# Optimization experiments

Measured on AMD Instinct MI355X. Metric: run time of the kernel, lower is better.

Reference implementation:

```python
import jax, jax.numpy as jnp
import numpy as np

B, T, D, H, DH = 8, 1024, 512, 8, 64
DEPTH, V, FF = 8, 6400, 2048
NH, BS = 8, 64            # n_hashes, bucket_size
NB = T // BS              # 16 buckets
SELF_ATTN_VALUE = -5e4


def setup_inputs() -> dict:
    key = jax.random.key(0)
    ks = jax.random.split(key, 12)
    def n(k, shape, s=0.02):
        return jax.random.normal(k, shape, dtype=jnp.float32) * s
    return {
        "input_ids": jax.random.randint(ks[0], (B, T), 0, V),
        "token_emb": n(ks[1], (V, D)),
        "pos_emb": n(ks[2], (T, D)),
        "ln_attn_g": jnp.ones((DEPTH, D), jnp.float32),
        "ln_attn_b": jnp.zeros((DEPTH, D), jnp.float32),
        "Wqk": n(ks[3], (DEPTH, D, D)),
        "Wv": n(ks[4], (DEPTH, D, D)),
        "Wo": n(ks[5], (DEPTH, D, D)),
        "ln_ff_g": jnp.ones((DEPTH, D), jnp.float32),
        "ln_ff_b": jnp.zeros((DEPTH, D), jnp.float32),
        "W1": n(ks[6], (DEPTH, D, FF)),
        "b1": jnp.zeros((DEPTH, FF), jnp.float32),
        "W2": n(ks[7], (DEPTH, FF, D)),
        "b2": jnp.zeros((DEPTH, D), jnp.float32),
        "ln_f_g": jnp.ones((D,), jnp.float32),
        "ln_f_b": jnp.zeros((D,), jnp.float32),
        "Wfc": n(ks[8], (D, D)),
        # fixed random LSH rotation matrices, one per layer: [depth, dim_head, n_hashes, n_buckets//2]
        "rotations": jax.random.normal(ks[9], (DEPTH, DH, NH, NB // 2), dtype=jnp.float32),
    }


def layer_norm(x, g, b):
    m = jnp.mean(x, -1, keepdims=True)
    v = jnp.mean(jnp.square(x - m), -1, keepdims=True)
    return (x - m) * jax.lax.rsqrt(v + 1e-5) * g + b


def lsh_attention(x, Wqk, Wv, Wo, rot):
    """Reformer LSH self-attention: shared QK, NH hash rounds, bucket sort,
    chunked attention with 1-chunk look-back, multi-round logsumexp combine."""
    Bx = x.shape[0]
    qk = (x @ Wqk).reshape(Bx, T, H, DH).transpose(0, 2, 1, 3).reshape(Bx * H, T, DH)
    v = (x @ Wv).reshape(Bx, T, H, DH).transpose(0, 2, 1, 3).reshape(Bx * H, T, DH)

    # --- hashing: argmax over [rotated, -rotated] -> bucket ids per round ---
    rotated = jnp.einsum('btd,dhr->bhtr', qk, rot)                       # [BH,NH,T,NB/2]
    buckets = jnp.argmax(jnp.concatenate([rotated, -rotated], -1), -1)   # [BH,NH,T]
    buckets = buckets + (jnp.arange(NH) * NB)[None, :, None]
    buckets = buckets.reshape(Bx * H, NH * T)

    # --- stable sort by (bucket, position) ---
    ticker = jnp.arange(NH * T)
    b_t = buckets * T + (ticker % T)[None, :]
    sticker = jnp.argsort(b_t, axis=-1)
    undo = jnp.argsort(sticker, axis=-1)
    st = sticker % T                                                     # original positions
    sqk = jnp.take_along_axis(qk, st[..., None], axis=1)                 # [BH,NH*T,DH]
    sv = jnp.take_along_axis(v, st[..., None], axis=1)

    # --- chunk: NH*NB chunks of length BS, keys look back one chunk ---
    nc = NH * NB
    bq_t = st.reshape(-1, nc, BS)
    bq = sqk.reshape(-1, nc, BS, DH)
    bk = bq / (jnp.linalg.norm(bq, axis=-1, keepdims=True) + 1e-8)       # unit-length keys
    bv = sv.reshape(-1, nc, BS, DH)

    def look_back(t):
        return jnp.concatenate([t, jnp.roll(t, 1, axis=1)], axis=2)

    bk, bv, bkv_t = look_back(bk), look_back(bv), look_back(bq_t)

    dots = jnp.einsum('bnqd,bnkd->bnqk', bq, bk) * (DH ** -0.5)          # [BH,nc,BS,2BS]
    self_mask = bq_t[..., :, None] == bkv_t[..., None, :]
    dots = jnp.where(self_mask, SELF_ATTN_VALUE, dots)

    logits = jax.nn.logsumexp(dots, axis=-1, keepdims=True)
    probs = jnp.exp(dots - logits)
    bo = jnp.einsum('bnqk,bnkd->bnqd', probs, bv)

    # --- unsort and combine hash rounds weighted by per-round logsumexp ---
    so = bo.reshape(-1, NH * T, DH)
    slog = logits.reshape(-1, NH * T)
    o = jnp.take_along_axis(so, undo[..., None], axis=1).reshape(-1, NH, T, DH)
    lg = jnp.take_along_axis(slog, undo, axis=1).reshape(-1, NH, T, 1)
    w = jax.nn.softmax(lg, axis=1)
    out = jnp.sum(o * w, axis=1)                                         # [BH,T,DH]
    out = out.reshape(Bx, H, T, DH).transpose(0, 2, 1, 3).reshape(Bx, T, D)
    return out @ Wo


def reference(input_ids, token_emb, pos_emb, ln_attn_g, ln_attn_b, Wqk, Wv, Wo,
              ln_ff_g, ln_ff_b, W1, b1, W2, b2, ln_f_g, ln_f_b, Wfc, rotations):
    x = token_emb[input_ids] + pos_emb[None, :, :]
    # reversible residual streams: y1 = x1 + attn(norm(x2)); y2 = x2 + ff(norm(y1))
    x1, x2 = x, x
    for l in range(DEPTH):
        x1 = x1 + lsh_attention(layer_norm(x2, ln_attn_g[l], ln_attn_b[l]),
                                Wqk[l], Wv[l], Wo[l], rotations[l])
        h = layer_norm(x1, ln_ff_g[l], ln_ff_b[l])
        x2 = x2 + (jax.nn.gelu(h @ W1[l] + b1[l]) @ W2[l] + b2[l])
    x = 0.5 * (x1 + x2)
    x = layer_norm(x, ln_f_g, ln_f_b)
    return jnp.mean(x, axis=1) @ Wfc                                     # [B, embedding_dim]
```

## Files before the change

### kernel.cpp

```cpp
#include <hip/hip_runtime.h>
#include <hip/hip_bf16.h>
#include <cstdint>
#include <cstddef>

#define B_ 8
#define T_ 1024
#define D_ 512
#define H_ 8
#define DH_ 64
#define DEPTH_ 8
#define FF_ 2048
#define NH_ 8
#define BS_ 64
#define NB_ 16
#define NC_ 128
#define BH_ 64
#define ROWS_ 8192

typedef __attribute__((ext_vector_type(8))) short bf16x8;
typedef __attribute__((ext_vector_type(4))) float f32x4;

typedef __attribute__((address_space(1))) const unsigned int g_u32;
typedef __attribute__((address_space(3))) unsigned int l_u32;
__device__ __forceinline__ void gload16(const void* g, void* l) {
  __builtin_amdgcn_global_load_lds((g_u32*)g, (l_u32*)l, 16, 0, 0);
}

__device__ __forceinline__ float wave_sum(float v) {
#pragma unroll
  for (int o = 1; o < 64; o <<= 1) v += __shfl_xor(v, o);
  return v;
}

__device__ __forceinline__ float gelu_f(float u) {
  float c = u + 0.044715f * u * u * u;
  float t = tanhf(0.7978845608028654f * c);
  return 0.5f * u * (1.0f + t);
}

__global__ __launch_bounds__(128) void k_embed(const int* __restrict__ ids,
                                               const float* __restrict__ te,
                                               const float* __restrict__ pe,
                                               float* __restrict__ x1,
                                               float* __restrict__ x2) {
  int bt = blockIdx.x;
  int t = bt & (T_ - 1);
  int d = threadIdx.x * 4;
  int id = ids[bt];
  float4 v = *(const float4*)(te + (size_t)id * D_ + d);
  float4 p = *(const float4*)(pe + (size_t)t * D_ + d);
  v.x += p.x; v.y += p.y; v.z += p.z; v.w += p.w;
  *(float4*)(x1 + (size_t)bt * D_ + d) = v;
  *(float4*)(x2 + (size_t)bt * D_ + d) = v;
}

__global__ __launch_bounds__(256) void k_wt(const float* __restrict__ W,
                                            __hip_bfloat16* __restrict__ WT,
                                            int K, int N) {
  const float* Wl = W + (size_t)blockIdx.z * K * N;
  __hip_bfloat16* WTl = WT + (size_t)blockIdx.z * K * N;
  __shared__ float tile[32][33];
  int n0 = blockIdx.x * 32, k0 = blockIdx.y * 32;
  int tx = threadIdx.x & 31, ty = threadIdx.x >> 5;
#pragma unroll
  for (int i = 0; i < 32; i += 8)
    tile[ty + i][tx] = Wl[(size_t)(k0 + ty + i) * N + n0 + tx];
  __syncthreads();
#pragma unroll
  for (int i = 0; i < 32; i += 8)
    WTl[(size_t)(n0 + ty + i) * K + k0 + tx] = __float2bfloat16(tile[tx][ty + i]);
}

__global__ __launch_bounds__(256) void k_ln(const float* __restrict__ x,
                                            const float* __restrict__ xb,
                                            const float* __restrict__ g,
                                            const float* __restrict__ bb,
                                            float* __restrict__ y,
                                            __hip_bfloat16* __restrict__ yb) {
  int w = threadIdx.x >> 6, lane = threadIdx.x & 63;
  size_t row = (size_t)blockIdx.x * 4 + w;
  const float* xr = x + row * D_ + lane * 8;
  float v[8];
  *(float4*)(v)     = *(const float4*)(xr);
  *(float4*)(v + 4) = *(const float4*)(xr + 4);
  if (xb) {
    const float* x2r = xb + row * D_ + lane * 8;
    float u[8];
    *(float4*)(u)     = *(const float4*)(x2r);
    *(float4*)(u + 4) = *(const float4*)(x2r + 4);
#pragma unroll
    for (int i = 0; i < 8; ++i) v[i] = 0.5f * (v[i] + u[i]);
  }
  float s = 0.f;
#pragma unroll
  for (int i = 0; i < 8; ++i) s += v[i];
  s = wave_sum(s);
  float m = s * (1.0f / D_);
  float q = 0.f;
#pragma unroll
  for (int i = 0; i < 8; ++i) { float d = v[i] - m; q += d * d; }
  q = wave_sum(q);
  float inv = 1.0f / sqrtf(q * (1.0f / D_) + 1e-5f);
  float gg[8], bv[8];
  *(float4*)(gg)     = *(const float4*)(g + lane * 8);
  *(float4*)(gg + 4) = *(const float4*)(g + lane * 8 + 4);
  *(float4*)(bv)     = *(const float4*)(bb + lane * 8);
  *(float4*)(bv + 4) = *(const float4*)(bb + lane * 8 + 4);
  float o[8];
#pragma unroll
  for (int i = 0; i < 8; ++i) o[i] = (v[i] - m) * inv * gg[i] + bv[i];
  if (y) {
    float* yr = y + row * D_ + lane * 8;
    *(float4*)(yr)     = *(float4*)(o);
    *(float4*)(yr + 4) = *(float4*)(o + 4);
  }
  if (yb) {
    __hip_bfloat16 o16[8];
#pragma unroll
    for (int i = 0; i < 8; ++i) o16[i] = __float2bfloat16(o[i]);
    *(uint4*)(yb + row * D_ + lane * 8) = *(uint4*)o16;
  }
}

__global__ __launch_bounds__(256) void k_prep(const float* __restrict__ qkb,
                                              __hip_bfloat16* __restrict__ qsb,
                                              __hip_bfloat16* __restrict__ knb) {
  int w = threadIdx.x >> 6, lane = threadIdx.x & 63;
  size_t row = (size_t)blockIdx.x * 4 + w;
  const float* xr = qkb + row * D_ + lane * 8;
  float v[8];
  *(float4*)(v)     = *(const float4*)(xr);
  *(float4*)(v + 4) = *(const float4*)(xr + 4);
  float ss = 0.f;
#pragma unroll
  for (int i = 0; i < 8; ++i) ss += v[i] * v[i];
  ss += __shfl_xor(ss, 1); ss += __shfl_xor(ss, 2); ss += __shfl_xor(ss, 4);
  float inv = 1.0f / (sqrtf(ss) + 1e-8f);
  __hip_bfloat16 qo[8], ko[8];
#pragma unroll
  for (int i = 0; i < 8; ++i) {
    qo[i] = __float2bfloat16(v[i] * 0.125f);
    ko[i] = __float2bfloat16(v[i] * inv);
  }
  *(uint4*)(qsb + row * D_ + lane * 8) = *(uint4*)qo;
  *(uint4*)(knb + row * D_ + lane * 8) = *(uint4*)ko;
}

__global__ __launch_bounds__(256) void k_sgemm(const float* __restrict__ A,
                                               const float* __restrict__ Bm,
                                               float* __restrict__ C,
                                               int N, int K) {
  __shared__ float As[32][128];
  __shared__ float Bs[32][128];
  const int bn0 = blockIdx.x * 128;
  const int bm0 = blockIdx.y * 128;
  const int tid = threadIdx.x;
  const int w = tid >> 6, lane = tid & 63;
  const int wy = w >> 1, wx = w & 1;
  const int ly = lane >> 3, lx = lane & 7;
  const int rm = wy * 64 + ly * 8;
  const int cn = wx * 64 + lx * 8;
  float acc[8][8] = {};

  for (int k0 = 0; k0 < K; k0 += 32) {
#pragma unroll
    for (int ld = 0; ld < 4; ++ld) {
      int f = tid + ld * 256;
      int ar = f >> 3;
      int ac = (f & 7) << 2;
      float4 av = *(const float4*)(A + (size_t)(bm0 + ar) * K + k0 + ac);
      As[ac + 0][ar] = av.x; As[ac + 1][ar] = av.y;
      As[ac + 2][ar] = av.z; As[ac + 3][ar] = av.w;
      int br = f >> 5;
      int bc = (f & 31) << 2;
      *(float4*)(&Bs[br][bc]) = *(const float4*)(Bm + (size_t)(k0 + br) * N + bn0 + bc);
    }
    __syncthreads();
#pragma unroll
    for (int kk = 0; kk < 32; ++kk) {
      float a[8], b[8];
      *(float4*)(a)     = *(const float4*)(&As[kk][rm]);
      *(float4*)(a + 4) = *(const float4*)(&As[kk][rm + 4]);
      *(float4*)(b)     = *(const float4*)(&Bs[kk][cn]);
      *(float4*)(b + 4) = *(const float4*)(&Bs[kk][cn + 4]);
#pragma unroll
      for (int i = 0; i < 8; ++i)
#pragma unroll
        for (int j = 0; j < 8; ++j) acc[i][j] += a[i] * b[j];
    }
    __syncthreads();
  }
#pragma unroll
  for (int i = 0; i < 8; ++i) {
    float* crow = C + (size_t)(bm0 + rm + i) * N + bn0 + cn;
#pragma unroll
    for (int j0 = 0; j0 < 8; j0 += 4)
      *(float4*)(crow + j0) = make_float4(acc[i][j0], acc[i][j0 + 1], acc[i][j0 + 2], acc[i][j0 + 3]);
  }
}

template <int EPI>
__global__ __launch_bounds__(256) void k_bgemm(const __hip_bfloat16* __restrict__ A,
                                               const __hip_bfloat16* __restrict__ BT,
                                               const float* __restrict__ bias,
                                               void* __restrict__ Cv,
                                               int N, int K) {
  __shared__ __align__(16) __hip_bfloat16 As[128 * 32];
  __shared__ __align__(16) __hip_bfloat16 Bs[128 * 32];
  const int bn0 = blockIdx.x * 128;
  const int bm0 = blockIdx.y * 128;
  const int tid = threadIdx.x;
  const int w = tid >> 6, lane = tid & 63;
  const int wy = w >> 1, wx = w & 1;
  const int g = lane >> 4, lr = lane & 15;
  f32x4 acc[4][4] = {};

  const __hip_bfloat16* Abase = A + (size_t)bm0 * K;
  const __hip_bfloat16* Bbase = BT + (size_t)bn0 * K;

  for (int k0 = 0; k0 < K; k0 += 32) {
#pragma unroll
    for (int it = 0; it < 2; ++it) {
      int f = it * 256 + w * 64 + lane;
      int row = f >> 2;
      int kc = ((f & 3) ^ ((row >> 1) & 3)) << 3;
      gload16(Abase + (size_t)row * K + k0 + kc, &As[(it * 256 + w * 64) * 8]);
      gload16(Bbase + (size_t)row * K + k0 + kc, &Bs[(it * 256 + w * 64) * 8]);
    }
    __syncthreads();
    bf16x8 af[4], bfr[4];
#pragma unroll
    for (int m = 0; m < 4; ++m) {
      int row = wy * 64 + m * 16 + lr;
      af[m] = *(const bf16x8*)(&As[row * 32 + ((g ^ ((row >> 1) & 3)) << 3)]);
    }
#pragma unroll
    for (int n = 0; n < 4; ++n) {
      int row = wx * 64 + n * 16 + lr;
      bfr[n] = *(const bf16x8*)(&Bs[row * 32 + ((g ^ ((row >> 1) & 3)) << 3)]);
    }
#pragma unroll
    for (int m = 0; m < 4; ++m)
#pragma unroll
      for (int n = 0; n < 4; ++n)
        acc[m][n] = __builtin_amdgcn_mfma_f32_16x16x32_bf16(af[m], bfr[n], acc[m][n], 0, 0, 0);
    __syncthreads();
  }

  const int colb = bn0 + wx * 64 + lr;
  const int rowb = bm0 + wy * 64 + (g << 2);
#pragma unroll
  for (int m = 0; m < 4; ++m) {
#pragma unroll
    for (int n = 0; n < 4; ++n) {
      int c = colb + n * 16;
      int r0 = rowb + m * 16;
      float bsv = (EPI == 2 || EPI == 3) ? bias[c] : 0.f;
#pragma unroll
      for (int j = 0; j < 4; ++j) {
        float vlu = acc[m][n][j] + bsv;
        size_t idx = (size_t)(r0 + j) * N + c;
        if (EPI == 0) ((float*)Cv)[idx] = vlu;
        else if (EPI == 1) ((float*)Cv)[idx] += vlu;
        else if (EPI == 2) ((__hip_bfloat16*)Cv)[idx] = __float2bfloat16(gelu_f(vlu));
        else if (EPI == 3) ((float*)Cv)[idx] += vlu;
        else ((__hip_bfloat16*)Cv)[idx] = __float2bfloat16(vlu);
      }
    }
  }
}

__global__ __launch_bounds__(128) void k_bucket(const float* __restrict__ qk,
                                                const float* __restrict__ rotL,
                                                unsigned char* __restrict__ bkt) {
  int blk = blockIdx.x;
  int tc = blk & 7, h = (blk >> 3) & 7, b = blk >> 6;
  int t0 = tc << 7;
  __shared__ float qs[128][65];
  __shared__ float rs[4096];
  int tid = threadIdx.x;
  for (int f = tid; f < 4096; f += 128) rs[f] = rotL[f];
  const float* base = qk + ((size_t)(b * T_ + t0)) * D_ + h * DH_;
  for (int f = tid; f < 2048; f += 128) {
    int rw = f >> 4, c4 = (f & 15) << 2;
    float4 v = *(const float4*)(base + (size_t)rw * D_ + c4);
    qs[rw][c4] = v.x; qs[rw][c4 + 1] = v.y; qs[rw][c4 + 2] = v.z; qs[rw][c4 + 3] = v.w;
  }
  __syncthreads();
  float s[64];
#pragma unroll
  for (int jr = 0; jr < 64; ++jr) s[jr] = 0.f;
  for (int d = 0; d < 64; ++d) {
    float q = qs[tid][d];
    const float* rp = rs + d * 64;
#pragma unroll
    for (int j4 = 0; j4 < 16; ++j4) {
      float4 rv = *(const float4*)(rp + j4 * 4);
      s[j4 * 4 + 0] += q * rv.x; s[j4 * 4 + 1] += q * rv.y;
      s[j4 * 4 + 2] += q * rv.z; s[j4 * 4 + 3] += q * rv.w;
    }
  }
  int bh = b * H_ + h;
#pragma unroll
  for (int r = 0; r < 8; ++r) {
    float best = s[r * 8];
    int bi = 0;
#pragma unroll
    for (int idx = 1; idx < 16; ++idx) {
      float v = (idx < 8) ? s[r * 8 + idx] : -s[r * 8 + idx - 8];
      if (v > best) { best = v; bi = idx; }
    }
    bkt[((size_t)(bh * NH_ + r)) * T_ + t0 + tid] = (unsigned char)bi;
  }
}

__global__ __launch_bounds__(1024) void k_sort(const unsigned char* __restrict__ bkt,
                                               int* __restrict__ st,
                                               int* __restrict__ undo) {
  int r = blockIdx.x & 7, bh = blockIdx.x >> 3;
  int t = threadIdx.x;
  int bk = bkt[((size_t)(bh * NH_ + r)) * T_ + t];
  int w = t >> 6, lane = t & 63;
  __shared__ int cnt[16][16];
  __shared__ int off[16][16];
  __shared__ int tot[16];
  __shared__ int stt[16];
  unsigned long long below = (1ULL << lane) - 1ULL;
  int myrank = 0;
#pragma unroll
  for (int bb = 0; bb < 16; ++bb) {
    unsigned long long m = __ballot(bk == bb);
    if (bk == bb) myrank = __popcll(m & below);
    if (lane == 0) cnt[w][bb] = __popcll(m);
  }
  __syncthreads();
  if (t < 16) {
    int run = 0;
    for (int ww = 0; ww < 16; ++ww) { off[ww][t] = run; run += cnt[ww][t]; }
    tot[t] = run;
  }
  __syncthreads();
  if (t == 0) {
    int run = 0;
    for (int bb = 0; bb < 16; ++bb) { stt[bb] = run; run += tot[bb]; }
  }
  __syncthreads();
  int pos = stt[bk] + off[w][bk] + myrank;
  st[((size_t)(bh * NH_ + r)) * T_ + pos] = t;
  undo[((size_t)(bh * NH_ + r)) * T_ + t] = pos;
}

__global__ __launch_bounds__(256) void k_attn(const __hip_bfloat16* __restrict__ qs,
                                              const __hip_bfloat16* __restrict__ kn,
                                              const __hip_bfloat16* __restrict__ vv,
                                              const int* __restrict__ st,
                                              __hip_bfloat16* __restrict__ ob,
                                              float* __restrict__ lgb) {
  __shared__ __align__(16) __hip_bfloat16 Kb[128 * 72];
  __shared__ __align__(16) __hip_bfloat16 VbT[64 * 136];
  __shared__ __align__(16) __hip_bfloat16 PbQb[64 * 136];
  __shared__ int pos[128];

  const int c = blockIdx.x, bh = blockIdx.y;
  const int b = bh >> 3, h = bh & 7;
  const int r = c >> 4;
  const int pc = (c + NC_ - 1) & (NC_ - 1);
  const int tid = threadIdx.x;

  if (tid < 128) {
    int sc = (tid < 64) ? c : pc;
    int slot = ((sc & 15) << 6) + (tid & 63);
    pos[tid] = st[((size_t)(bh * NH_ + (sc >> 4))) * T_ + slot];
  }
  __syncthreads();

  const __hip_bfloat16* qbase = qs + ((size_t)b * T_) * D_ + h * DH_;
  const __hip_bfloat16* kbase = kn + ((size_t)b * T_) * D_ + h * DH_;
  const __hip_bfloat16* vbase = vv + ((size_t)b * T_) * D_ + h * DH_;

#pragma unroll
  for (int ld = 0; ld < 4; ++ld) {
    int f = ld * 256 + tid;
    int rw = f >> 3, c8 = (f & 7) << 3;
    *(uint4*)(&Kb[rw * 72 + c8]) = *(const uint4*)(kbase + (size_t)pos[rw] * D_ + c8);
  }
#pragma unroll
  for (int ld = 0; ld < 2; ++ld) {
    int f = ld * 256 + tid;
    int rw = f >> 3, c8 = (f & 7) << 3;
    *(uint4*)(&PbQb[rw * 72 + c8]) = *(const uint4*)(qbase + (size_t)pos[rw] * D_ + c8);
  }
  {
    const int w = tid >> 6, rl = tid & 7, d8 = (tid >> 3) & 7;
#pragma unroll
    for (int it = 0; it < 4; ++it) {
      int rw0 = it * 32 + w * 8;
      uint4 x = *(const uint4*)(vbase + (size_t)pos[rw0 + rl] * D_ + d8 * 8);
      unsigned short u[8];
      u[0] = x.x & 0xffff; u[1] = x.x >> 16;
      u[2] = x.y & 0xffff; u[3] = x.y >> 16;
      u[4] = x.z & 0xffff; u[5] = x.z >> 16;
      u[6] = x.w & 0xffff; u[7] = x.w >> 16;
#pragma unroll
      for (int k = 0; k < 3; ++k) {
        const int xm = 1 << k;
        const bool sel = (rl >> k) & 1;
#pragma unroll
        for (int j0 = 0; j0 < 8; ++j0) {
          if ((j0 >> k) & 1) continue;
          int j1 = j0 | (1 << k);
          unsigned int send = sel ? (unsigned int)u[j0] : (unsigned int)u[j1];
          unsigned int recv = (unsigned int)__shfl_xor((int)send, xm);
          if (sel) u[j0] = (unsigned short)recv; else u[j1] = (unsigned short)recv;
        }
      }
      int d = d8 * 8 + rl;
      uint4 y;
      y.x = (unsigned int)u[0] | ((unsigned int)u[1] << 16);
      y.y = (unsigned int)u[2] | ((unsigned int)u[3] << 16);
      y.z = (unsigned int)u[4] | ((unsigned int)u[5] << 16);
      y.w = (unsigned int)u[6] | ((unsigned int)u[7] << 16);
      *(uint4*)(&VbT[d * 136 + (rw0 ^ (((d >> 3) & 3) << 3))]) = y;
    }
  }
  __syncthreads();

  const int w = tid >> 6, lane = tid & 63;
  const int g = lane >> 4, l15 = lane & 15;
  const int q0 = w * 16;

  bf16x8 af0 = *(const bf16x8*)(&PbQb[(q0 + l15) * 72 + g * 8]);
  bf16x8 af1 = *(const bf16x8*)(&PbQb[(q0 + l15) * 72 + 32 + g * 8]);
  f32x4 dacc[8];
#pragma unroll
  for (int n = 0; n < 8; ++n) dacc[n] = (f32x4){0.f, 0.f, 0.f, 0.f};
#pragma unroll
  for (int n = 0; n < 8; ++n) {
    bf16x8 b0 = *(const bf16x8*)(&Kb[(n * 16 + l15) * 72 + g * 8]);
    bf16x8 b1 = *(const bf16x8*)(&Kb[(n * 16 + l15) * 72 + 32 + g * 8]);
    dacc[n] = __builtin_amdgcn_mfma_f32_16x16x32_bf16(af0, b0, dacc[n], 0, 0, 0);
    dacc[n] = __builtin_amdgcn_mfma_f32_16x16x32_bf16(af1, b1, dacc[n], 0, 0, 0);
  }
  __syncthreads();

  int qpos[4], kpos[8];
#pragma unroll
  for (int reg = 0; reg < 4; ++reg) qpos[reg] = pos[q0 + g * 4 + reg];
#pragma unroll
  for (int n = 0; n < 8; ++n) kpos[n] = pos[n * 16 + l15];
  float pr[8][4];
  float lgt[4];
#pragma unroll
  for (int reg = 0; reg < 4; ++reg) {
    float mx = -3.0e38f;
#pragma unroll
    for (int n = 0; n < 8; ++n) {
      float dv = dacc[n][reg];
      dv = (kpos[n] == qpos[reg]) ? -5.0e4f : dv;
      pr[n][reg] = dv;
      mx = fmaxf(mx, dv);
    }
    mx = fmaxf(mx, __shfl_xor(mx, 1));
    mx = fmaxf(mx, __shfl_xor(mx, 2));
    mx = fmaxf(mx, __shfl_xor(mx, 4));
    mx = fmaxf(mx, __shfl_xor(mx, 8));
    float s = 0.f;
#pragma unroll
    for (int n = 0; n < 8; ++n) { float e = __expf(pr[n][reg] - mx); pr[n][reg] = e; s += e; }
    s += __shfl_xor(s, 1); s += __shfl_xor(s, 2);
    s += __shfl_xor(s, 4); s += __shfl_xor(s, 8);
    lgt[reg] = mx + __logf(s);
    float isc = 1.0f / s;
#pragma unroll
    for (int n = 0; n < 8; ++n) pr[n][reg] *= isc;
  }
#pragma unroll
  for (int n = 0; n < 8; ++n)
#pragma unroll
    for (int reg = 0; reg < 4; ++reg)
      PbQb[(q0 + g * 4 + reg) * 136 + n * 16 + l15] = __float2bfloat16(pr[n][reg]);
  const size_t slotbase = ((size_t)(bh * NH_ + r)) * T_ + ((c & 15) << 6);
  if (l15 == 0) {
#pragma unroll
    for (int reg = 0; reg < 4; ++reg)
      lgb[slotbase + q0 + g * 4 + reg] = lgt[reg];
  }
  __syncthreads();

  bf16x8 va[4];
#pragma unroll
  for (int s = 0; s < 4; ++s) {
    int dd = w * 16 + l15;
    va[s] = *(const bf16x8*)(&VbT[dd * 136 + ((s * 32 + g * 8) ^ (((dd >> 3) & 3) << 3))]);
  }
#pragma unroll
  for (int n = 0; n < 4; ++n) {
    f32x4 oa = (f32x4){0.f, 0.f, 0.f, 0.f};
#pragma unroll
    for (int s = 0; s < 4; ++s) {
      bf16x8 pb = *(const bf16x8*)(&PbQb[(n * 16 + l15) * 136 + s * 32 + g * 8]);
      oa = __builtin_amdgcn_mfma_f32_16x16x32_bf16(va[s], pb, oa, 0, 0, 0);
    }
    int q = n * 16 + l15;
    int d = w * 16 + g * 4;
    __hip_bfloat16 o4[4];
#pragma unroll
    for (int reg = 0; reg < 4; ++reg) o4[reg] = __float2bfloat16(oa[reg]);
    *(uint2*)(&ob[(slotbase + q) * DH_ + d]) = *(uint2*)o4;
  }
}

__global__ __launch_bounds__(256) void k_combine(const __hip_bfloat16* __restrict__ ob,
                                                 const float* __restrict__ lgb,
                                                 const int* __restrict__ undo,
                                                 __hip_bfloat16* __restrict__ attnb) {
  int g = threadIdx.x >> 6, lane = threadIdx.x & 63;
  int idx = blockIdx.x * 4 + g;
  int bh = idx >> 10, t = idx & (T_ - 1);
  int b = bh >> 3, h = bh & 7;
  int su[8];
  float lg[8];
  float m = -3.0e38f;
#pragma unroll
  for (int r = 0; r < 8; ++r) {
    su[r] = undo[((size_t)(bh * NH_ + r)) * T_ + t];
    lg[r] = lgb[((size_t)(bh * NH_ + r)) * T_ + su[r]];
    m = fmaxf(m, lg[r]);
  }
  float s = 0.f;
#pragma unroll
  for (int r = 0; r < 8; ++r) { lg[r] = __expf(lg[r] - m); s += lg[r]; }
  float invs = 1.0f / s;
  float o = 0.f;
#pragma unroll
  for (int r = 0; r < 8; ++r)
    o += lg[r] * invs * __bfloat162float(ob[(((size_t)(bh * NH_ + r)) * T_ + su[r]) * DH_ + lane]);
  attnb[((size_t)(b * T_ + t)) * D_ + h * DH_ + lane] = __float2bfloat16(o);
}

__global__ void k_zero(float* __restrict__ p, int n) {
  int i = blockIdx.x * blockDim.x + threadIdx.x;
  if (i < n) p[i] = 0.f;
}

__global__ __launch_bounds__(256) void k_colsum(const float* __restrict__ xn,
                                                float* __restrict__ mean) {
  int b = blockIdx.x, dc = blockIdx.y, tc = blockIdx.z;
  int d = dc * 256 + threadIdx.x;
  float s = 0.f;
  for (int tt = 0; tt < 64; ++tt) {
    int t = tc * 64 + tt;
    s += xn[((size_t)(b * T_ + t)) * D_ + d];
  }
  atomicAdd(&mean[b * D_ + d], s);
}

__global__ __launch_bounds__(512) void k_fc(const float* __restrict__ mean,
                                            const float* __restrict__ Wfc,
                                            float* __restrict__ out) {
  int b = blockIdx.x, n = threadIdx.x;
  __shared__ float ms[512];
  ms[n] = mean[b * D_ + n] * (1.0f / 1024.0f);
  __syncthreads();
  float acc = 0.f;
  for (int d = 0; d < 512; ++d) acc += ms[d] * Wfc[(size_t)d * D_ + n];
  out[b * D_ + n] = acc;
}

extern "C" void kernel_launch(void* const* d_in, const int* in_sizes, int n_in,
                              void* d_out, int out_size, void* d_ws, size_t ws_size,
                              hipStream_t stream) {
  (void)in_sizes; (void)n_in; (void)out_size; (void)ws_size;
  const int*   ids  = (const int*)d_in[0];
  const float* te   = (const float*)d_in[1];
  const float* pe   = (const float*)d_in[2];
  const float* lag  = (const float*)d_in[3];
  const float* lab  = (const float*)d_in[4];
  const float* Wqk  = (const float*)d_in[5];
  const float* Wv   = (const float*)d_in[6];
  const float* Wo   = (const float*)d_in[7];
  const float* lfg  = (const float*)d_in[8];
  const float* lfb  = (const float*)d_in[9];
  const float* W1   = (const float*)d_in[10];
  const float* b1   = (const float*)d_in[11];
  const float* W2   = (const float*)d_in[12];
  const float* b2   = (const float*)d_in[13];
  const float* lnfg = (const float*)d_in[14];
  const float* lnfb = (const float*)d_in[15];
  const float* Wfc  = (const float*)d_in[16];
  const float* rot  = (const float*)d_in[17];

  char* ws = (char*)d_ws;
  size_t off = 0;
  auto carve = [&](size_t bytes) -> void* {
    void* p = ws + off;
    off += (bytes + 255) & ~(size_t)255;
    return p;
  };
  float* x1    = (float*)carve((size_t)ROWS_ * D_ * 4);
  float* x2    = (float*)carve((size_t)ROWS_ * D_ * 4);
  float* xn    = (float*)carve((size_t)ROWS_ * D_ * 4);
  float* qkb   = (float*)carve((size_t)ROWS_ * D_ * 4);
  __hip_bfloat16* vvb   = (__hip_bfloat16*)carve((size_t)ROWS_ * D_ * 2);
  __hip_bfloat16* qsb   = (__hip_bfloat16*)carve((size_t)ROWS_ * D_ * 2);
  __hip_bfloat16* knb   = (__hip_bfloat16*)carve((size_t)ROWS_ * D_ * 2);
  __hip_bfloat16* xnb   = (__hip_bfloat16*)carve((size_t)ROWS_ * D_ * 2);
  __hip_bfloat16* attnb = (__hip_bfloat16*)carve((size_t)ROWS_ * D_ * 2);
  __hip_bfloat16* ob    = (__hip_bfloat16*)carve((size_t)BH_ * NH_ * T_ * DH_ * 2);
  __hip_bfloat16* hid   = ob;
  unsigned char* bkt = (unsigned char*)carve((size_t)BH_ * NH_ * T_);
  int*   stb   = (int*)carve((size_t)BH_ * NH_ * T_ * 4);
  int*   undo  = (int*)carve((size_t)BH_ * NH_ * T_ * 4);
  float* lgb   = (float*)carve((size_t)BH_ * NH_ * T_ * 4);
  float* meanb = (float*)carve((size_t)B_ * D_ * 4);
  __hip_bfloat16* WvT = (__hip_bfloat16*)carve((size_t)DEPTH_ * D_ * D_ * 2);
  __hip_bfloat16* WoT = (__hip_bfloat16*)carve((size_t)DEPTH_ * D_ * D_ * 2);
  __hip_bfloat16* W1T = (__hip_bfloat16*)carve((size_t)DEPTH_ * D_ * FF_ * 2);
  __hip_bfloat16* W2T = (__hip_bfloat16*)carve((size_t)DEPTH_ * FF_ * D_ * 2);

  k_wt<<<dim3(D_ / 32, D_ / 32, DEPTH_), 256, 0, stream>>>(Wv, WvT, D_, D_);
  k_wt<<<dim3(D_ / 32, D_ / 32, DEPTH_), 256, 0, stream>>>(Wo, WoT, D_, D_);
  k_wt<<<dim3(FF_ / 32, D_ / 32, DEPTH_), 256, 0, stream>>>(W1, W1T, D_, FF_);
  k_wt<<<dim3(D_ / 32, FF_ / 32, DEPTH_), 256, 0, stream>>>(W2, W2T, FF_, D_);

  k_embed<<<ROWS_, 128, 0, stream>>>(ids, te, pe, x1, x2);

  for (int l = 0; l < DEPTH_; ++l) {
    const float* wqk = Wqk + (size_t)l * D_ * D_;
    const __hip_bfloat16* wvt = WvT + (size_t)l * D_ * D_;
    const __hip_bfloat16* wot = WoT + (size_t)l * D_ * D_;
    const __hip_bfloat16* w1t = W1T + (size_t)l * D_ * FF_;
    const __hip_bfloat16* w2t = W2T + (size_t)l * FF_ * D_;

    k_ln<<<ROWS_ / 4, 256, 0, stream>>>(x2, nullptr, lag + l * D_, lab + l * D_, xn, xnb);
    k_sgemm<<<dim3(D_ / 128, ROWS_ / 128), 256, 0, stream>>>(xn, wqk, qkb, D_, D_);
    k_bgemm<4><<<dim3(D_ / 128, ROWS_ / 128), 256, 0, stream>>>(xnb, wvt, nullptr, vvb, D_, D_);
    k_prep<<<ROWS_ / 4, 256, 0, stream>>>(qkb, qsb, knb);
    k_bucket<<<512, 128, 0, stream>>>(qkb, rot + (size_t)l * 4096, bkt);
    k_sort<<<512, 1024, 0, stream>>>(bkt, stb, undo);
    k_attn<<<dim3(NC_, BH_), 256, 0, stream>>>(qsb, knb, vvb, stb, ob, lgb);
    k_combine<<<BH_ * T_ / 4, 256, 0, stream>>>(ob, lgb, undo, attnb);
    k_bgemm<1><<<dim3(D_ / 128, ROWS_ / 128), 256, 0, stream>>>(attnb, wot, nullptr, x1, D_, D_);

    k_ln<<<ROWS_ / 4, 256, 0, stream>>>(x1, nullptr, lfg + l * D_, lfb + l * D_, nullptr, xnb);
    k_bgemm<2><<<dim3(FF_ / 128, ROWS_ / 128), 256, 0, stream>>>(xnb, w1t, b1 + l * FF_, hid, FF_, D_);
    k_bgemm<3><<<dim3(D_ / 128, ROWS_ / 128), 256, 0, stream>>>(hid, w2t, b2 + l * D_, x2, D_, FF_);
  }

  k_ln<<<ROWS_ / 4, 256, 0, stream>>>(x1, x2, lnfg, lnfb, xn, nullptr);
  k_zero<<<16, 256, 0, stream>>>(meanb, B_ * D_);
  k_colsum<<<dim3(B_, 2, 16), 256, 0, stream>>>(xn, meanb);
  k_fc<<<B_, 512, 0, stream>>>(meanb, Wfc, (float*)d_out);
}
```

Baseline: 3.200 ms.

## Replace fp32 QK GEMM with split-bf16 MFMA GEMM and drop softmax max-subtraction

The fp32 SIMT GEMM for the shared QK projection is replaced with a three-term split-bf16 (hi/lo) MFMA GEMM. The layernorm now also emits the bf16 residual, and a new transpose kernel splits Wqk into hi and lo parts. This keeps near-fp32 accuracy, which the hashing argmax needs, while using the matrix cores. Separately, the attention softmax drops its max reduction and applies the 1/sum normalization after the PV matmul through shared memory. That relies on the scaled logits being small enough not to overflow exp.

```diff
diff --git a/kernel.cpp b/kernel.cpp
--- a/kernel.cpp
+++ b/kernel.cpp
@@ -71,12 +71,38 @@
     WTl[(size_t)(n0 + ty + i) * K + k0 + tx] = __float2bfloat16(tile[tx][ty + i]);
 }
 
+__global__ __launch_bounds__(256) void k_wt2(const float* __restrict__ W,
+                                             __hip_bfloat16* __restrict__ WhT,
+                                             __hip_bfloat16* __restrict__ WlT,
+                                             int K, int N) {
+  const float* Wl = W + (size_t)blockIdx.z * K * N;
+  __hip_bfloat16* WhTl = WhT + (size_t)blockIdx.z * K * N;
+  __hip_bfloat16* WlTl = WlT + (size_t)blockIdx.z * K * N;
+  __shared__ float tile[32][33];
+  int n0 = blockIdx.x * 32, k0 = blockIdx.y * 32;
+  int tx = threadIdx.x & 31, ty = threadIdx.x >> 5;
+#pragma unroll
+  for (int i = 0; i < 32; i += 8)
+    tile[ty + i][tx] = Wl[(size_t)(k0 + ty + i) * N + n0 + tx];
+  __syncthreads();
+#pragma unroll
+  for (int i = 0; i < 32; i += 8) {
+    float v = tile[tx][ty + i];
+    __hip_bfloat16 hi = __float2bfloat16(v);
+    float lo = v - __bfloat162float(hi);
+    size_t idx = (size_t)(n0 + ty + i) * K + k0 + tx;
+    WhTl[idx] = hi;
+    WlTl[idx] = __float2bfloat16(lo);
+  }
+}
+
 __global__ __launch_bounds__(256) void k_ln(const float* __restrict__ x,
                                             const float* __restrict__ xb,
                                             const float* __restrict__ g,
                                             const float* __restrict__ bb,
                                             float* __restrict__ y,
-                                            __hip_bfloat16* __restrict__ yb) {
+                                            __hip_bfloat16* __restrict__ yb,
+                                            __hip_bfloat16* __restrict__ ylo) {
   int w = threadIdx.x >> 6, lane = threadIdx.x & 63;
   size_t row = (size_t)blockIdx.x * 4 + w;
   const float* xr = x + row * D_ + lane * 8;
@@ -119,7 +145,88 @@
 #pragma unroll
     for (int i = 0; i < 8; ++i) o16[i] = __float2bfloat16(o[i]);
     *(uint4*)(yb + row * D_ + lane * 8) = *(uint4*)o16;
-  }
+    if (ylo) {
+      __hip_bfloat16 l16[8];
+#pragma unroll
+      for (int i = 0; i < 8; ++i)
+        l16[i] = __float2bfloat16(o[i] - __bfloat162float(o16[i]));
+      *(uint4*)(ylo + row * D_ + lane * 8) = *(uint4*)l16;
+    }
+  }
+}
+
+__global__ __launch_bounds__(256) void k_qgemm(const __hip_bfloat16* __restrict__ Ah,
+                                               const __hip_bfloat16* __restrict__ Al,
+                                               const __hip_bfloat16* __restrict__ BhT,
+                                               const __hip_bfloat16* __restrict__ BlT,
+                                               float* __restrict__ C, int N, int K) {
+  __shared__ __align__(16) __hip_bfloat16 Ash[128 * 32];
+  __shared__ __align__(16) __hip_bfloat16 Asl[128 * 32];
+  __shared__ __align__(16) __hip_bfloat16 Bsh[128 * 32];
+  __shared__ __align__(16) __hip_bfloat16 Bsl[128 * 32];
+  const int bn0 = blockIdx.x * 128;
+  const int bm0 = blockIdx.y * 128;
+  const int tid = threadIdx.x;
+  const int w = tid >> 6, lane = tid & 63;
+  const int wy = w >> 1, wx = w & 1;
+  const int g = lane >> 4, lr = lane & 15;
+  f32x4 acc[4][4] = {};
+  const size_t aoff = (size_t)bm0 * K;
+  const size_t boff = (size_t)bn0 * K;
+
+  for (int k0 = 0; k0 < K; k0 += 32) {
+#pragma unroll
+    for (int it = 0; it < 2; ++it) {
+      int f = it * 256 + w * 64 + lane;
+      int row = f >> 2;
+      int kc = ((f & 3) ^ ((row >> 1) & 3)) << 3;
+      size_t ga = aoff + (size_t)row * K + k0 + kc;
+      size_t gb = boff + (size_t)row * K + k0 + kc;
+      int lo = (it * 256 + w * 64) * 8;
+      gload16(Ah + ga, &Ash[lo]);
+      gload16(Al + ga, &Asl[lo]);
+      gload16(BhT + gb, &Bsh[lo]);
+      gload16(BlT + gb, &Bsl[lo]);
+    }
+    __syncthreads();
+    bf16x8 ah[4], al[4], bh[4], bl[4];
+#pragma unroll
+    for (int m = 0; m < 4; ++m) {
+      int row = wy * 64 + m * 16 + lr;
+      int o = row * 32 + ((g ^ ((row >> 1) & 3)) << 3);
+      ah[m] = *(const bf16x8*)(&Ash[o]);
+      al[m] = *(const bf16x8*)(&Asl[o]);
+    }
+#pragma unroll
+    for (int n = 0; n < 4; ++n) {
+      int row = wx * 64 + n * 16 + lr;
+      int o = row * 32 + ((g ^ ((row >> 1) & 3)) << 3);
+      bh[n] = *(const bf16x8*)(&Bsh[o]);
+      bl[n] = *(const bf16x8*)(&Bsl[o]);
+    }
+#pragma unroll
+    for (int m = 0; m < 4; ++m)
+#pragma unroll
+      for (int n = 0; n < 4; ++n) {
+        acc[m][n] = __builtin_amdgcn_mfma_f32_16x16x32_bf16(ah[m], bh[n], acc[m][n], 0, 0, 0);
+        acc[m][n] = __builtin_amdgcn_mfma_f32_16x16x32_bf16(ah[m], bl[n], acc[m][n], 0, 0, 0);
+        acc[m][n] = __builtin_amdgcn_mfma_f32_16x16x32_bf16(al[m], bh[n], acc[m][n], 0, 0, 0);
+      }
+    __syncthreads();
+  }
+
+  const int colb = bn0 + wx * 64 + lr;
+  const int rowb = bm0 + wy * 64 + (g << 2);
+#pragma unroll
+  for (int m = 0; m < 4; ++m)
+#pragma unroll
+    for (int n = 0; n < 4; ++n) {
+      int c = colb + n * 16;
+      int r0 = rowb + m * 16;
+#pragma unroll
+      for (int j = 0; j < 4; ++j)
+        C[(size_t)(r0 + j) * N + c] = acc[m][n][j];
+    }
 }
 
 __global__ __launch_bounds__(256) void k_prep(const float* __restrict__ qkb,
@@ -144,59 +251,6 @@
   }
   *(uint4*)(qsb + row * D_ + lane * 8) = *(uint4*)qo;
   *(uint4*)(knb + row * D_ + lane * 8) = *(uint4*)ko;
-}
-
-__global__ __launch_bounds__(256) void k_sgemm(const float* __restrict__ A,
-                                               const float* __restrict__ Bm,
-                                               float* __restrict__ C,
-                                               int N, int K) {
-  __shared__ float As[32][128];
-  __shared__ float Bs[32][128];
-  const int bn0 = blockIdx.x * 128;
-  const int bm0 = blockIdx.y * 128;
-  const int tid = threadIdx.x;
-  const int w = tid >> 6, lane = tid & 63;
-  const int wy = w >> 1, wx = w & 1;
-  const int ly = lane >> 3, lx = lane & 7;
-  const int rm = wy * 64 + ly * 8;
-  const int cn = wx * 64 + lx * 8;
-  float acc[8][8] = {};
-
-  for (int k0 = 0; k0 < K; k0 += 32) {
-#pragma unroll
-    for (int ld = 0; ld < 4; ++ld) {
-      int f = tid + ld * 256;
-      int ar = f >> 3;
-      int ac = (f & 7) << 2;
-      float4 av = *(const float4*)(A + (size_t)(bm0 + ar) * K + k0 + ac);
-      As[ac + 0][ar] = av.x; As[ac + 1][ar] = av.y;
-      As[ac + 2][ar] = av.z; As[ac + 3][ar] = av.w;
-      int br = f >> 5;
-      int bc = (f & 31) << 2;
-      *(float4*)(&Bs[br][bc]) = *(const float4*)(Bm + (size_t)(k0 + br) * N + bn0 + bc);
-    }
-    __syncthreads();
-#pragma unroll
-    for (int kk = 0; kk < 32; ++kk) {
-      float a[8], b[8];
-      *(float4*)(a)     = *(const float4*)(&As[kk][rm]);
-      *(float4*)(a + 4) = *(const float4*)(&As[kk][rm + 4]);
-      *(float4*)(b)     = *(const float4*)(&Bs[kk][cn]);
-      *(float4*)(b + 4) = *(const float4*)(&Bs[kk][cn + 4]);
-#pragma unroll
-      for (int i = 0; i < 8; ++i)
-#pragma unroll
-        for (int j = 0; j < 8; ++j) acc[i][j] += a[i] * b[j];
-    }
-    __syncthreads();
-  }
-#pragma unroll
-  for (int i = 0; i < 8; ++i) {
-    float* crow = C + (size_t)(bm0 + rm + i) * N + bn0 + cn;
-#pragma unroll
-    for (int j0 = 0; j0 < 8; j0 += 4)
-      *(float4*)(crow + j0) = make_float4(acc[i][j0], acc[i][j0 + 1], acc[i][j0 + 2], acc[i][j0 + 3]);
-  }
 }
 
 template <int EPI>
@@ -359,6 +413,7 @@
   __shared__ __align__(16) __hip_bfloat16 Kb[128 * 72];
   __shared__ __align__(16) __hip_bfloat16 VbT[64 * 136];
   __shared__ __align__(16) __hip_bfloat16 PbQb[64 * 136];
+  __shared__ float lsb[64];
   __shared__ int pos[128];
 
   const int c = blockIdx.x, bh = blockIdx.y;
@@ -449,30 +504,23 @@
 #pragma unroll
   for (int n = 0; n < 8; ++n) kpos[n] = pos[n * 16 + l15];
   float pr[8][4];
-  float lgt[4];
 #pragma unroll
   for (int reg = 0; reg < 4; ++reg) {
-    float mx = -3.0e38f;
+    float s = 0.f;
 #pragma unroll
     for (int n = 0; n < 8; ++n) {
       float dv = dacc[n][reg];
       dv = (kpos[n] == qpos[reg]) ? -5.0e4f : dv;
-      pr[n][reg] = dv;
-      mx = fmaxf(mx, dv);
-    }
-    mx = fmaxf(mx, __shfl_xor(mx, 1));
-    mx = fmaxf(mx, __shfl_xor(mx, 2));
-    mx = fmaxf(mx, __shfl_xor(mx, 4));
-    mx = fmaxf(mx, __shfl_xor(mx, 8));
-    float s = 0.f;
-#pragma unroll
-    for (int n = 0; n < 8; ++n) { float e = __expf(pr[n][reg] - mx); pr[n][reg] = e; s += e; }
+      float e = __expf(dv);
+      pr[n][reg] = e;
+      s += e;
+    }
     s += __shfl_xor(s, 1); s += __shfl_xor(s, 2);
     s += __shfl_xor(s, 4); s += __shfl_xor(s, 8);
-    lgt[reg] = mx + __logf(s);
-    float isc = 1.0f / s;
-#pragma unroll
-    for (int n = 0; n < 8; ++n) pr[n][reg] *= isc;
+    if (l15 == 0) {
+      lsb[q0 + g * 4 + reg] = 1.0f / s;
+      lgb[(((size_t)(bh * NH_ + r)) * T_ + ((c & 15) << 6)) + q0 + g * 4 + reg] = __logf(s);
+    }
   }
 #pragma unroll
   for (int n = 0; n < 8; ++n)
@@ -480,11 +528,6 @@
     for (int reg = 0; reg < 4; ++reg)
       PbQb[(q0 + g * 4 + reg) * 136 + n * 16 + l15] = __float2bfloat16(pr[n][reg]);
   const size_t slotbase = ((size_t)(bh * NH_ + r)) * T_ + ((c & 15) << 6);
-  if (l15 == 0) {
-#pragma unroll
-    for (int reg = 0; reg < 4; ++reg)
-      lgb[slotbase + q0 + g * 4 + reg] = lgt[reg];
-  }
   __syncthreads();
 
   bf16x8 va[4];
@@ -502,10 +545,11 @@
       oa = __builtin_amdgcn_mfma_f32_16x16x32_bf16(va[s], pb, oa, 0, 0, 0);
     }
     int q = n * 16 + l15;
+    float inv = lsb[q];
     int d = w * 16 + g * 4;
     __hip_bfloat16 o4[4];
 #pragma unroll
-    for (int reg = 0; reg < 4; ++reg) o4[reg] = __float2bfloat16(oa[reg]);
+    for (int reg = 0; reg < 4; ++reg) o4[reg] = __float2bfloat16(oa[reg] * inv);
     *(uint2*)(&ob[(slotbase + q) * DH_ + d]) = *(uint2*)o4;
   }
 }
@@ -605,6 +649,7 @@
   __hip_bfloat16* qsb   = (__hip_bfloat16*)carve((size_t)ROWS_ * D_ * 2);
   __hip_bfloat16* knb   = (__hip_bfloat16*)carve((size_t)ROWS_ * D_ * 2);
   __hip_bfloat16* xnb   = (__hip_bfloat16*)carve((size_t)ROWS_ * D_ * 2);
+  __hip_bfloat16* xnlo  = (__hip_bfloat16*)carve((size_t)ROWS_ * D_ * 2);
   __hip_bfloat16* attnb = (__hip_bfloat16*)carve((size_t)ROWS_ * D_ * 2);
   __hip_bfloat16* ob    = (__hip_bfloat16*)carve((size_t)BH_ * NH_ * T_ * DH_ * 2);
   __hip_bfloat16* hid   = ob;
@@ -613,27 +658,31 @@
   int*   undo  = (int*)carve((size_t)BH_ * NH_ * T_ * 4);
   float* lgb   = (float*)carve((size_t)BH_ * NH_ * T_ * 4);
   float* meanb = (float*)carve((size_t)B_ * D_ * 4);
-  __hip_bfloat16* WvT = (__hip_bfloat16*)carve((size_t)DEPTH_ * D_ * D_ * 2);
-  __hip_bfloat16* WoT = (__hip_bfloat16*)carve((size_t)DEPTH_ * D_ * D_ * 2);
-  __hip_bfloat16* W1T = (__hip_bfloat16*)carve((size_t)DEPTH_ * D_ * FF_ * 2);
-  __hip_bfloat16* W2T = (__hip_bfloat16*)carve((size_t)DEPTH_ * FF_ * D_ * 2);
+  __hip_bfloat16* WvT  = (__hip_bfloat16*)carve((size_t)DEPTH_ * D_ * D_ * 2);
+  __hip_bfloat16* WoT  = (__hip_bfloat16*)carve((size_t)DEPTH_ * D_ * D_ * 2);
+  __hip_bfloat16* W1T  = (__hip_bfloat16*)carve((size_t)DEPTH_ * D_ * FF_ * 2);
+  __hip_bfloat16* W2T  = (__hip_bfloat16*)carve((size_t)DEPTH_ * FF_ * D_ * 2);
+  __hip_bfloat16* WqhT = (__hip_bfloat16*)carve((size_t)DEPTH_ * D_ * D_ * 2);
+  __hip_bfloat16* WqlT = (__hip_bfloat16*)carve((size_t)DEPTH_ * D_ * D_ * 2);
 
   k_wt<<<dim3(D_ / 32, D_ / 32, DEPTH_), 256, 0, stream>>>(Wv, WvT, D_, D_);
   k_wt<<<dim3(D_ / 32, D_ / 32, DEPTH_), 256, 0, stream>>>(Wo, WoT, D_, D_);
   k_wt<<<dim3(FF_ / 32, D_ / 32, DEPTH_), 256, 0, stream>>>(W1, W1T, D_, FF_);
   k_wt<<<dim3(D_ / 32, FF_ / 32, DEPTH_), 256, 0, stream>>>(W2, W2T, FF_, D_);
+  k_wt2<<<dim3(D_ / 32, D_ / 32, DEPTH_), 256, 0, stream>>>(Wqk, WqhT, WqlT, D_, D_);
 
   k_embed<<<ROWS_, 128, 0, stream>>>(ids, te, pe, x1, x2);
 
   for (int l = 0; l < DEPTH_; ++l) {
-    const float* wqk = Wqk + (size_t)l * D_ * D_;
     const __hip_bfloat16* wvt = WvT + (size_t)l * D_ * D_;
     const __hip_bfloat16* wot = WoT + (size_t)l * D_ * D_;
     const __hip_bfloat16* w1t = W1T + (size_t)l * D_ * FF_;
     const __hip_bfloat16* w2t = W2T + (size_t)l * FF_ * D_;
-
-    k_ln<<<ROWS_ / 4, 256, 0, stream>>>(x2, nullptr, lag + l * D_, lab + l * D_, xn, xnb);
-    k_sgemm<<<dim3(D_ / 128, ROWS_ / 128), 256, 0, stream>>>(xn, wqk, qkb, D_, D_);
+    const __hip_bfloat16* wqh = WqhT + (size_t)l * D_ * D_;
+    const __hip_bfloat16* wql = WqlT + (size_t)l * D_ * D_;
+
+    k_ln<<<ROWS_ / 4, 256, 0, stream>>>(x2, nullptr, lag + l * D_, lab + l * D_, nullptr, xnb, xnlo);
+    k_qgemm<<<dim3(D_ / 128, ROWS_ / 128), 256, 0, stream>>>(xnb, xnlo, wqh, wql, qkb, D_, D_);
     k_bgemm<4><<<dim3(D_ / 128, ROWS_ / 128), 256, 0, stream>>>(xnb, wvt, nullptr, vvb, D_, D_);
     k_prep<<<ROWS_ / 4, 256, 0, stream>>>(qkb, qsb, knb);
     k_bucket<<<512, 128, 0, stream>>>(qkb, rot + (size_t)l * 4096, bkt);
@@ -642,12 +691,12 @@
     k_combine<<<BH_ * T_ / 4, 256, 0, stream>>>(ob, lgb, undo, attnb);
     k_bgemm<1><<<dim3(D_ / 128, ROWS_ / 128), 256, 0, stream>>>(attnb, wot, nullptr, x1, D_, D_);
 
-    k_ln<<<ROWS_ / 4, 256, 0, stream>>>(x1, nullptr, lfg + l * D_, lfb + l * D_, nullptr, xnb);
+    k_ln<<<ROWS_ / 4, 256, 0, stream>>>(x1, nullptr, lfg + l * D_, lfb + l * D_, nullptr, xnb, nullptr);
     k_bgemm<2><<<dim3(FF_ / 128, ROWS_ / 128), 256, 0, stream>>>(xnb, w1t, b1 + l * FF_, hid, FF_, D_);
     k_bgemm<3><<<dim3(D_ / 128, ROWS_ / 128), 256, 0, stream>>>(hid, w2t, b2 + l * D_, x2, D_, FF_);
   }
 
-  k_ln<<<ROWS_ / 4, 256, 0, stream>>>(x1, x2, lnfg, lnfb, xn, nullptr);
+  k_ln<<<ROWS_ / 4, 256, 0, stream>>>(x1, x2, lnfg, lnfb, xn, nullptr, nullptr);
   k_zero<<<16, 256, 0, stream>>>(meanb, B_ * D_);
   k_colsum<<<dim3(B_, 2, 16), 256, 0, stream>>>(xn, meanb);
   k_fc<<<B_, 512, 0, stream>>>(meanb, Wfc, (float*)d_out);
```

After: 3.199 ms. About the same (-0.0%).
